# Kernel tuning notes

Measured on AMD Instinct MI355X. Metric: run time of the kernel, lower is better.

Reference implementation:

```python
import jax, jax.numpy as jnp
import numpy as np

N, K, H = 98, 10, 4        # landmarks, neighbors/node, heads
B, CIN, HC = 1024, 256, 64 # batch, in_channels, head_channels
NEG = -9e15


def setup_inputs() -> dict:
    key = jax.random.key(0)
    ks = jax.random.split(key, 3)
    rng = np.random.default_rng(0)
    # fixed sparsity pattern: K unique neighbors per row, row-major order
    cols2d = np.stack([np.sort(rng.choice(N, K, replace=False)) for _ in range(N)])
    rows = np.repeat(np.arange(N), K)
    cols = cols2d.reshape(-1)
    x = jax.random.normal(ks[0], (B, N, CIN), jnp.float32)
    W = jax.random.normal(ks[1], (H, 2, CIN, HC), jnp.float32) * 0.05  # xavier-ish
    e = jnp.ones((H, N * K), jnp.float32)  # nn.init.constant_(e, 1)
    stdv = 1.0 / np.sqrt(HC)
    bias = jax.random.uniform(ks[2], (H, HC), jnp.float32, -stdv, stdv)
    return {"x": x, "W": W, "e": e, "bias": bias,
            "rows": jnp.asarray(rows, jnp.int32),
            "cols": jnp.asarray(cols, jnp.int32)}


def reference(x, W, e, bias, rows, cols):
    # h0/h1 for all heads at once: [2, H, B, N, HC]
    h = jnp.einsum('bnc,hscd->shbnd', x, W)
    h0, h1 = h[0], h[1]
    # masked adjacency logits per head: -9e15 everywhere, learned e at edges
    base = jnp.full((N, N), NEG, jnp.float32)
    logits = jax.vmap(lambda eh: base.at[rows, cols].set(eh))(e)  # [H,N,N]
    A = jax.nn.softmax(logits, axis=-1)  # F.softmax(adj, dim=1) on [N,N]
    diag = jnp.diagonal(A, axis1=-2, axis2=-1)  # [H,N] -> adj*M part
    A_off = A - diag[..., None] * jnp.eye(N, dtype=A.dtype)  # adj*(1-M)
    out = diag[:, None, :, None] * h0 + jnp.einsum('hij,hbjd->hbid', A_off, h1)
    out = out + bias[:, None, None, :]  # [H,B,N,HC]
    # concat heads along channel dim -> [B, N, H*HC]
    return jnp.transpose(out, (1, 2, 0, 3)).reshape(B, N, H * HC)
```

## Files before the change

### kernel.cpp

```cpp
#include <hip/hip_runtime.h>

typedef __bf16 bf16;
typedef bf16 bf16x4 __attribute__((ext_vector_type(4)));
typedef bf16 bf16x8 __attribute__((ext_vector_type(8)));
typedef float f32x4 __attribute__((ext_vector_type(4)));

#define NND 98
#define KNB 10
#define NH 4
#define CIN 256
#define HC 64
#define XROW_B 528
#define CROW_E 140

__global__ __launch_bounds__(256) void prep_wp_kernel(const float* __restrict__ W,
                                                      bf16* __restrict__ Wp) {
  int t = blockIdx.x * 256 + threadIdx.x;
  if (t >= 8 * 8 * 4 * 64) return;
  int lane = t & 63;
  int nt = (t >> 6) & 3;
  int kt = (t >> 8) & 7;
  int hs = t >> 11;
  int n = nt * 16 + (lane & 15);
  int kb = kt * 32 + (lane >> 4) * 8;
  const float* src = W + (hs * CIN + kb) * HC + n;
  bf16x8 v;
#pragma unroll
  for (int j = 0; j < 8; ++j) v[j] = (bf16)src[j * HC];
  *(bf16x8*)(Wp + (long long)t * 8) = v;
}

__global__ __launch_bounds__(256, 2) void semgconv_kernel(
    const float* __restrict__ x, const float* __restrict__ e,
    const float* __restrict__ bias, const int* __restrict__ cols,
    const bf16* __restrict__ Wp, float* __restrict__ out, int B) {
  __shared__ __align__(16) unsigned char reg0[112 * XROW_B];
  __shared__ float w_lds[NND * KNB];
  __shared__ short cols_lds[NND * KNB];
  __shared__ float diag_lds[NND];

  const int tid = threadIdx.x;
  const int bid = blockIdx.x;
  const int b = bid >> 2;
  const int h = bid & 3;

  if (tid < NND) {
    const int i = tid;
    const float* ep = e + (h * NND + i) * KNB;
    const int* cp = cols + i * KNB;
    float ev[KNB]; int cv[KNB];
    float mx = -3.0e38f;
#pragma unroll
    for (int j = 0; j < KNB; ++j) { ev[j] = ep[j]; cv[j] = cp[j]; mx = fmaxf(mx, ev[j]); }
    float s = 0.f;
#pragma unroll
    for (int j = 0; j < KNB; ++j) { ev[j] = __expf(ev[j] - mx); s += ev[j]; }
    const float inv = 1.f / s;
    float dg = 0.f;
#pragma unroll
    for (int j = 0; j < KNB; ++j) {
      float wvv = ev[j] * inv;
      if (cv[j] == i) { dg = wvv; wvv = 0.f; }
      w_lds[i * KNB + j] = wvv;
      cols_lds[i * KNB + j] = (short)cv[j];
    }
    diag_lds[i] = dg;
  }

  {
    const float* xb = x + (long long)b * NND * CIN;
#pragma unroll
    for (int it = 0; it < 28; ++it) {
      int idx = tid + it * 256;
      int n = idx >> 6;
      int c4 = (idx & 63) << 2;
      f32x4 v = {0.f, 0.f, 0.f, 0.f};
      if (n < NND) v = *(const f32x4*)(xb + n * CIN + c4);
      bf16x4 bv;
      bv[0] = (bf16)v[0]; bv[1] = (bf16)v[1]; bv[2] = (bf16)v[2]; bv[3] = (bf16)v[3];
      *(bf16x4*)(reg0 + n * XROW_B + c4 * 2) = bv;
    }
  }
  __syncthreads();

  const int lane = tid & 63;
  const int wv = tid >> 6;
  const int wn = wv & 1;
  const int wm = wv >> 1;
  const int mt0 = wm * 4;

  f32x4 acc[4][4] = {};
  const unsigned char* aptr = reg0 + (mt0 * 16 + (lane & 15)) * XROW_B + (lane >> 4) * 16;
  const bf16* wpl = Wp + ((long long)((h * 2 + wn) * 8 * 4 * 64) + lane) * 8;

#pragma unroll
  for (int kt = 0; kt < 8; ++kt) {
    bf16x8 bfr[4];
#pragma unroll
    for (int p = 0; p < 4; ++p)
      bfr[p] = *(const bf16x8*)(wpl + (kt * 4 + p) * 64 * 8);
    bf16x8 afr[4];
#pragma unroll
    for (int im = 0; im < 4; ++im)
      if (mt0 + im < 7)
        afr[im] = *(const bf16x8*)(aptr + im * (16 * XROW_B) + kt * 64);
#pragma unroll
    for (int im = 0; im < 4; ++im)
      if (mt0 + im < 7) {
#pragma unroll
        for (int p = 0; p < 4; ++p)
          acc[im][p] =
              __builtin_amdgcn_mfma_f32_16x16x32_bf16(afr[im], bfr[p], acc[im][p], 0, 0, 0);
      }
  }
  __syncthreads();

  {
    bf16* C = (bf16*)reg0;
#pragma unroll
    for (int im = 0; im < 4; ++im)
      if (mt0 + im < 7) {
        int rowb = (mt0 + im) * 16 + (lane >> 4) * 4;
#pragma unroll
        for (int p = 0; p < 4; ++p) {
          int col = (wn * 4 + p) * 16 + (lane & 15);
#pragma unroll
          for (int r = 0; r < 4; ++r)
            C[(rowb + r) * CROW_E + col] = (bf16)acc[im][p][r];
        }
      }
  }
  __syncthreads();

  {
    const bf16* C = (const bf16*)reg0;
    const int ig = tid >> 4;
    const int d4 = (tid & 15) * 4;
    f32x4 bs = *(const f32x4*)(bias + h * HC + d4);
    float* outp = out + (long long)b * NND * (NH * HC) + h * HC + d4;
#pragma unroll
    for (int ib = 0; ib < 7; ++ib) {
      int i = ib * 16 + ig;
      if (i < NND) {
        f32x4 av = bs;
        float dg = diag_lds[i];
        bf16x4 c0 = *(const bf16x4*)(C + i * CROW_E + d4);
        av[0] += dg * (float)c0[0];
        av[1] += dg * (float)c0[1];
        av[2] += dg * (float)c0[2];
        av[3] += dg * (float)c0[3];
#pragma unroll
        for (int j = 0; j < KNB; ++j) {
          float wj = w_lds[i * KNB + j];
          int cj = cols_lds[i * KNB + j];
          bf16x4 c1 = *(const bf16x4*)(C + cj * CROW_E + HC + d4);
          av[0] += wj * (float)c1[0];
          av[1] += wj * (float)c1[1];
          av[2] += wj * (float)c1[2];
          av[3] += wj * (float)c1[3];
        }
        *(f32x4*)(outp + (long long)i * (NH * HC)) = av;
      }
    }
  }
}

extern "C" void kernel_launch(void* const* d_in, const int* in_sizes, int n_in,
                              void* d_out, int out_size, void* d_ws, size_t ws_size,
                              hipStream_t stream) {
  const float* x    = (const float*)d_in[0];
  const float* W    = (const float*)d_in[1];
  const float* e    = (const float*)d_in[2];
  const float* bias = (const float*)d_in[3];
  const int* cols   = (const int*)d_in[5];
  float* out        = (float*)d_out;
  bf16* Wp          = (bf16*)d_ws;

  int B = in_sizes[0] / (NND * CIN);

  prep_wp_kernel<<<64, 256, 0, stream>>>(W, Wp);
  semgconv_kernel<<<B * NH, 256, 0, stream>>>(x, e, bias, cols, Wp, out, B);
}
```

Measured before the change: 267.4 us.

## Process all heads per batch block to load and convert x once

Each block now handles one batch element with 1024 threads instead of one (batch, head) pair with 256 threads, so x is read from global memory and converted to bf16 once instead of four times. Each of the 16 waves computes a 2-m-tile by 8-n-tile slice of the GEMM for a single head. The heads are then processed one after another through the shared C buffer: the owning waves write their tile and all threads do the sparse aggregation. This removes the redundant x traffic but adds a serialized per-head loop with two barriers each, recomputes the softmax weights inside that loop, and raises register pressure at 1024 threads per block. The C-buffer row pitch also changes from 140 to 136.

```diff
diff --git a/kernel.cpp b/kernel.cpp
--- a/kernel.cpp
+++ b/kernel.cpp
@@ -11,7 +11,7 @@
 #define CIN 256
 #define HC 64
 #define XROW_B 528
-#define CROW_E 140
+#define CROW_E 136
 
 __global__ __launch_bounds__(256) void prep_wp_kernel(const float* __restrict__ W,
                                                       bf16* __restrict__ Wp) {
@@ -30,48 +30,29 @@
   *(bf16x8*)(Wp + (long long)t * 8) = v;
 }
 
-__global__ __launch_bounds__(256, 2) void semgconv_kernel(
+__global__ __launch_bounds__(1024, 4) void semgconv_kernel(
     const float* __restrict__ x, const float* __restrict__ e,
     const float* __restrict__ bias, const int* __restrict__ cols,
-    const bf16* __restrict__ Wp, float* __restrict__ out, int B) {
+    const bf16* __restrict__ Wp, float* __restrict__ out) {
   __shared__ __align__(16) unsigned char reg0[112 * XROW_B];
   __shared__ float w_lds[NND * KNB];
   __shared__ short cols_lds[NND * KNB];
   __shared__ float diag_lds[NND];
 
   const int tid = threadIdx.x;
-  const int bid = blockIdx.x;
-  const int b = bid >> 2;
-  const int h = bid & 3;
+  const int b = blockIdx.x;
 
   if (tid < NND) {
-    const int i = tid;
-    const float* ep = e + (h * NND + i) * KNB;
-    const int* cp = cols + i * KNB;
-    float ev[KNB]; int cv[KNB];
-    float mx = -3.0e38f;
-#pragma unroll
-    for (int j = 0; j < KNB; ++j) { ev[j] = ep[j]; cv[j] = cp[j]; mx = fmaxf(mx, ev[j]); }
-    float s = 0.f;
-#pragma unroll
-    for (int j = 0; j < KNB; ++j) { ev[j] = __expf(ev[j] - mx); s += ev[j]; }
-    const float inv = 1.f / s;
-    float dg = 0.f;
-#pragma unroll
-    for (int j = 0; j < KNB; ++j) {
-      float wvv = ev[j] * inv;
-      if (cv[j] == i) { dg = wvv; wvv = 0.f; }
-      w_lds[i * KNB + j] = wvv;
-      cols_lds[i * KNB + j] = (short)cv[j];
-    }
-    diag_lds[i] = dg;
+    const int* cp = cols + tid * KNB;
+#pragma unroll
+    for (int j = 0; j < KNB; ++j) cols_lds[tid * KNB + j] = (short)cp[j];
   }
 
   {
     const float* xb = x + (long long)b * NND * CIN;
 #pragma unroll
-    for (int it = 0; it < 28; ++it) {
-      int idx = tid + it * 256;
+    for (int it = 0; it < 7; ++it) {
+      int idx = tid + it * 1024;
       int n = idx >> 6;
       int c4 = (idx & 63) << 2;
       f32x4 v = {0.f, 0.f, 0.f, 0.f};
@@ -85,83 +66,122 @@
 
   const int lane = tid & 63;
   const int wv = tid >> 6;
-  const int wn = wv & 1;
-  const int wm = wv >> 1;
-  const int mt0 = wm * 4;
-
-  f32x4 acc[4][4] = {};
+  const int wh = wv & 3;
+  const int wm = wv >> 2;
+  const int mt0 = wm * 2;
+
+  f32x4 acc[2][8] = {};
   const unsigned char* aptr = reg0 + (mt0 * 16 + (lane & 15)) * XROW_B + (lane >> 4) * 16;
-  const bf16* wpl = Wp + ((long long)((h * 2 + wn) * 8 * 4 * 64) + lane) * 8;
+  const bf16* wpl = Wp + ((long long)(wh * 2) * (8 * 4 * 64) + lane) * 8;
 
 #pragma unroll
   for (int kt = 0; kt < 8; ++kt) {
-    bf16x8 bfr[4];
-#pragma unroll
-    for (int p = 0; p < 4; ++p)
-      bfr[p] = *(const bf16x8*)(wpl + (kt * 4 + p) * 64 * 8);
-    bf16x8 afr[4];
-#pragma unroll
-    for (int im = 0; im < 4; ++im)
+    bf16x8 afr[2];
+#pragma unroll
+    for (int im = 0; im < 2; ++im)
       if (mt0 + im < 7)
         afr[im] = *(const bf16x8*)(aptr + im * (16 * XROW_B) + kt * 64);
-#pragma unroll
-    for (int im = 0; im < 4; ++im)
-      if (mt0 + im < 7) {
-#pragma unroll
-        for (int p = 0; p < 4; ++p)
-          acc[im][p] =
-              __builtin_amdgcn_mfma_f32_16x16x32_bf16(afr[im], bfr[p], acc[im][p], 0, 0, 0);
+    {
+      bf16x8 bfr[4];
+#pragma unroll
+      for (int nt = 0; nt < 4; ++nt)
+        bfr[nt] = *(const bf16x8*)(wpl + ((kt * 4 + nt) * 64) * 8);
+#pragma unroll
+      for (int im = 0; im < 2; ++im)
+        if (mt0 + im < 7)
+#pragma unroll
+          for (int nt = 0; nt < 4; ++nt)
+            acc[im][nt] = __builtin_amdgcn_mfma_f32_16x16x32_bf16(afr[im], bfr[nt],
+                                                                  acc[im][nt], 0, 0, 0);
+    }
+    {
+      bf16x8 bfr[4];
+#pragma unroll
+      for (int nt = 0; nt < 4; ++nt)
+        bfr[nt] = *(const bf16x8*)(wpl + ((8 * 4 + kt * 4 + nt) * 64) * 8);
+#pragma unroll
+      for (int im = 0; im < 2; ++im)
+        if (mt0 + im < 7)
+#pragma unroll
+          for (int nt = 0; nt < 4; ++nt)
+            acc[im][4 + nt] = __builtin_amdgcn_mfma_f32_16x16x32_bf16(afr[im], bfr[nt],
+                                                                      acc[im][4 + nt], 0, 0, 0);
+    }
+  }
+  __syncthreads();
+
+  bf16* C = (bf16*)reg0;
+  const int ig = tid >> 4;
+  const int d4 = (tid & 15) * 4;
+
+  for (int h = 0; h < NH; ++h) {
+    if (tid < NND) {
+      const int i = tid;
+      const float* ep = e + (h * NND + i) * KNB;
+      float ev[KNB];
+      float mx = -3.0e38f;
+#pragma unroll
+      for (int j = 0; j < KNB; ++j) { ev[j] = ep[j]; mx = fmaxf(mx, ev[j]); }
+      float s = 0.f;
+#pragma unroll
+      for (int j = 0; j < KNB; ++j) { ev[j] = __expf(ev[j] - mx); s += ev[j]; }
+      const float inv = 1.f / s;
+      float dg = 0.f;
+#pragma unroll
+      for (int j = 0; j < KNB; ++j) {
+        float wvv = ev[j] * inv;
+        if ((int)cols_lds[i * KNB + j] == i) { dg = wvv; wvv = 0.f; }
+        w_lds[i * KNB + j] = wvv;
       }
-  }
-  __syncthreads();
-
-  {
-    bf16* C = (bf16*)reg0;
-#pragma unroll
-    for (int im = 0; im < 4; ++im)
-      if (mt0 + im < 7) {
-        int rowb = (mt0 + im) * 16 + (lane >> 4) * 4;
-#pragma unroll
-        for (int p = 0; p < 4; ++p) {
-          int col = (wn * 4 + p) * 16 + (lane & 15);
-#pragma unroll
-          for (int r = 0; r < 4; ++r)
-            C[(rowb + r) * CROW_E + col] = (bf16)acc[im][p][r];
+      diag_lds[i] = dg;
+    }
+    if (wh == h) {
+#pragma unroll
+      for (int im = 0; im < 2; ++im) {
+        int mt = mt0 + im;
+        if (mt < 7) {
+          int rowb = mt * 16 + (lane >> 4) * 4;
+#pragma unroll
+          for (int q = 0; q < 8; ++q) {
+            int col = q * 16 + (lane & 15);
+#pragma unroll
+            for (int r = 0; r < 4; ++r)
+              C[(rowb + r) * CROW_E + col] = (bf16)acc[im][q][r];
+          }
         }
       }
-  }
-  __syncthreads();
-
-  {
-    const bf16* C = (const bf16*)reg0;
-    const int ig = tid >> 4;
-    const int d4 = (tid & 15) * 4;
-    f32x4 bs = *(const f32x4*)(bias + h * HC + d4);
-    float* outp = out + (long long)b * NND * (NH * HC) + h * HC + d4;
-#pragma unroll
-    for (int ib = 0; ib < 7; ++ib) {
-      int i = ib * 16 + ig;
-      if (i < NND) {
-        f32x4 av = bs;
-        float dg = diag_lds[i];
-        bf16x4 c0 = *(const bf16x4*)(C + i * CROW_E + d4);
-        av[0] += dg * (float)c0[0];
-        av[1] += dg * (float)c0[1];
-        av[2] += dg * (float)c0[2];
-        av[3] += dg * (float)c0[3];
-#pragma unroll
-        for (int j = 0; j < KNB; ++j) {
-          float wj = w_lds[i * KNB + j];
-          int cj = cols_lds[i * KNB + j];
-          bf16x4 c1 = *(const bf16x4*)(C + cj * CROW_E + HC + d4);
-          av[0] += wj * (float)c1[0];
-          av[1] += wj * (float)c1[1];
-          av[2] += wj * (float)c1[2];
-          av[3] += wj * (float)c1[3];
+    }
+    __syncthreads();
+
+    {
+      f32x4 bs = *(const f32x4*)(bias + h * HC + d4);
+      float* outp = out + (long long)b * NND * (NH * HC) + h * HC + d4;
+#pragma unroll
+      for (int ib = 0; ib < 2; ++ib) {
+        int i = ib * 64 + ig;
+        if (i < NND) {
+          f32x4 av = bs;
+          float dg = diag_lds[i];
+          bf16x4 c0 = *(const bf16x4*)(C + i * CROW_E + d4);
+          av[0] += dg * (float)c0[0];
+          av[1] += dg * (float)c0[1];
+          av[2] += dg * (float)c0[2];
+          av[3] += dg * (float)c0[3];
+#pragma unroll
+          for (int j = 0; j < KNB; ++j) {
+            float wj = w_lds[i * KNB + j];
+            int cj = (int)cols_lds[i * KNB + j];
+            bf16x4 c1 = *(const bf16x4*)(C + cj * CROW_E + HC + d4);
+            av[0] += wj * (float)c1[0];
+            av[1] += wj * (float)c1[1];
+            av[2] += wj * (float)c1[2];
+            av[3] += wj * (float)c1[3];
+          }
+          *(f32x4*)(outp + (long long)i * (NH * HC)) = av;
         }
-        *(f32x4*)(outp + (long long)i * (NH * HC)) = av;
       }
     }
+    __syncthreads();
   }
 }
 
@@ -179,5 +199,5 @@
   int B = in_sizes[0] / (NND * CIN);
 
   prep_wp_kernel<<<64, 256, 0, stream>>>(W, Wp);
-  semgconv_kernel<<<B * NH, 256, 0, stream>>>(x, e, bias, cols, Wp, out, B);
+  semgconv_kernel<<<B, 1024, 0, stream>>>(x, e, bias, cols, Wp, out);
 }
```

Result: faster. 257.8 us (-3.6%).
